# Kernel optimization log

Measured on AMD Instinct MI355X. Metric: run time of the kernel, lower is better.

## Reference

```python
import math
import jax, jax.numpy as jnp
import numpy as np

B, C_IN, H, W = 32, 96, 64, 64
OUT = 128
EXC = int(OUT * 0.8)   # 102 excitatory channels
INH = OUT - EXC        # 26 inhibitory channels
K = 5
PAD = 2                # kernel//2 so all stages keep spatial size


def _sm_kernel(kernel_size=5, sigma_e=1.2, sigma_i=1.4):
    c = kernel_size // 2
    xx, yy = np.meshgrid(np.arange(kernel_size), np.arange(kernel_size), indexing='ij')
    xx = xx.astype(np.float32) - c
    yy = yy.astype(np.float32) - c
    ge = np.exp(-(xx ** 2 + yy ** 2) / (2 * sigma_e ** 2))
    gi = np.exp(-(xx ** 2 + yy ** 2) / (2 * sigma_i ** 2))
    dog = ge / (2 * math.pi * sigma_e ** 2) - gi / (2 * math.pi * sigma_i ** 2)
    dog = dog / dog[c, c]
    return jnp.asarray(dog[None, None], dtype=jnp.float32)  # [1,1,K,K]


def setup_inputs() -> dict:
    key = jax.random.key(0)
    k1, k2, k3, k4 = jax.random.split(key, 4)
    wr = 25.0 / math.sqrt(C_IN * K * K)
    x = jax.random.normal(k1, (B, C_IN, H, W), jnp.float32)
    w_ee = wr * jnp.abs(jax.random.normal(k2, (EXC, C_IN, K, K), jnp.float32))
    w_ei = wr * jnp.abs(jax.random.normal(k3, (INH, EXC, K, K), jnp.float32))
    w_ie = -wr * jnp.abs(jax.random.normal(k4, (EXC, INH, K, K), jnp.float32))
    return {"x": x, "w_ee": w_ee, "w_ei": w_ei, "w_ie": w_ie, "sm_kernel": _sm_kernel()}


def _reflect_pad(x, p):
    if p == 0:
        return x
    return jnp.pad(x, ((0, 0), (0, 0), (p, p), (p, p)), mode='reflect')


def _conv(x, w, pad=0, groups=1):
    return jax.lax.conv_general_dilated(
        x, w, window_strides=(1, 1), padding=[(pad, pad), (pad, pad)],
        dimension_numbers=('NCHW', 'OIHW', 'NCHW'), feature_group_count=groups)


def _forward(x, w_ee, w_ei, w_ie, sm_kernel):
    y_e = _conv(_reflect_pad(x, PAD), w_ee)                 # [B,EXC,H,W], act=Identity
    y_i = jax.nn.relu(_conv(_reflect_pad(y_e, PAD), w_ei))  # [B,INH,H,W]
    y_ie = _conv(_reflect_pad(y_i, PAD), w_ie)              # [B,EXC,H,W]
    y = y_e + y_ie
    # depthwise surround-modulation conv (zero padding, as in F.conv2d)
    w_sm = jnp.tile(sm_kernel, (EXC, 1, 1, 1))              # [EXC,1,K,K]
    y = _conv(y, w_sm, pad=K // 2, groups=EXC)
    return y, y_e, y_i


def reference(x, w_ee, w_ei, w_ie, sm_kernel):
    y, y_e, y_i = _forward(x, w_ee, w_ei, w_ie, sm_kernel)

    # --- hard WTA masks (winner channel per (b,h,w) position) ---
    win_e = jnp.argmax(y_e, axis=1)                                        # [B,H,W]
    mask_e = (jnp.arange(EXC)[None, :, None, None] == win_e[:, None]).astype(y_e.dtype)
    y_wta_e = y_e * mask_e
    win_i = jnp.argmax(jnp.abs(y_i), axis=1)
    mask_i = (jnp.arange(INH)[None, :, None, None] == win_i[:, None]).astype(y_i.dtype)
    y_wta_i = y_i * mask_i

    # --- transpose-conv outer-product trick; with same-size feature maps the
    # conv collapses to a 1x1 full correlation over (b,h,w) -> einsum ---
    yx_ee = jnp.einsum('bchw,behw->ec', x, y_wta_e)[:, :, None, None]      # [EXC,C_IN,1,1]
    yx_ei = jnp.einsum('behw,bihw->ie', y_wta_e, y_wta_i)[:, :, None, None]  # [INH,EXC,1,1]
    yx_ie = jnp.einsum('bihw,behw->ei', y_wta_i, y)[:, :, None, None]      # [EXC,INH,1,1]

    yu_e = jnp.sum(y_wta_e, axis=(0, 2, 3))[:, None, None, None]           # [EXC,1,1,1]
    yu_i = jnp.sum(jnp.abs(y_wta_i), axis=(0, 2, 3))[:, None, None, None]  # [INH,1,1,1]

    upd_ee = yx_ee - yu_e * w_ee   # broadcasts to [EXC,C_IN,K,K]
    upd_ei = yx_ei - yu_i * w_ei
    upd_ie = yx_ie - yu_e * w_ie
    upd_ee = upd_ee / (jnp.abs(upd_ee).max() + 1e-8)
    upd_ei = upd_ei / (jnp.abs(upd_ei).max() + 1e-8)
    upd_ie = upd_ie / (jnp.abs(upd_ie).max() + 1e-8)

    return (y, upd_ee, upd_ei, upd_ie)
```

## Files before the change

### kernel.cpp

```cpp
#include <hip/hip_runtime.h>

#define B_    32
#define CIN_  96
#define EXC_  102
#define INH_  26
#define HH    64
#define WW    64
#define HW_   4096
#define NPOS  (B_*HW_)
#define EEPAD 97
#define NPART 1024
#define NEE   (EXC_*CIN_ + EXC_)
#define NIE   (EXC_*INH_)
#define N1U   (EXC_*CIN_*25)
#define N2U   (INH_*EXC_*25)
#define N3U   (EXC_*INH_*25)

typedef short bf8 __attribute__((ext_vector_type(8)));
typedef float f32x4 __attribute__((ext_vector_type(4)));

__device__ __forceinline__ int refl(int i) {
    if (i < 0) i = -i;
    if (i > 63) i = 126 - i;
    return i;
}

__device__ __forceinline__ short f2bf(float f) {
    unsigned u = __float_as_uint(f);
    return (short)((u + 0x7fffu + ((u >> 16) & 1u)) >> 16);
}

__global__ __launch_bounds__(256) void pack_all(
    const float* __restrict__ w_ee, const float* __restrict__ w_ei,
    const float* __restrict__ w_ie, const float* __restrict__ x,
    short* __restrict__ wdst, short* __restrict__ xdst,
    float* __restrict__ zreg)
{
    const int blk = blockIdx.x;
    if (blk < 1800) {
        int gi = blk*256 + threadIdx.x;
        if (gi >= 460800) return;
        const float* src; int N, C, NPAD, CPAD; int idx;
        if (gi < 268800)      { src = w_ee; N = 102; C = 96;  NPAD = 112; CPAD = 96;  idx = gi; }
        else if (gi < 371200) { src = w_ei; N = 26;  C = 102; NPAD = 32;  CPAD = 128; idx = gi - 268800; }
        else                  { src = w_ie; N = 102; C = 26;  NPAD = 112; CPAD = 32;  idx = gi - 371200; }
        int tap = idx / (NPAD*CPAD);
        int rem = idx - tap*(NPAD*CPAD);
        int n = rem / CPAD, c = rem - n*CPAD;
        float f = (n < N && c < C) ? src[((size_t)n*C + c)*25 + tap] : 0.f;
        wdst[gi] = f2bf(f);
    } else if (blk < 3848) {
        int bb = blk - 1800;
        int b = bb >> 6, bx = bb & 63;
        const int pos = bx*64 + (threadIdx.x & 63);
        const int cg0 = threadIdx.x >> 6;
        for (int cg = cg0; cg < 96/8; cg += 4) {
            bf8 v;
#pragma unroll
            for (int j = 0; j < 8; ++j)
                v[j] = f2bf(x[((size_t)b*CIN_ + cg*8 + j)*HW_ + pos]);
            *(bf8*)(&xdst[((size_t)b*HW_ + pos)*96 + cg*8]) = v;
        }
    } else {
        for (int i = threadIdx.x; i < INH_*EXC_ + INH_ + 3; i += 256) zreg[i] = 0.f;
    }
}

template<int C, int CPAD>
__global__ __launch_bounds__(256) void pack_nhwc(
    const float* __restrict__ src, short* __restrict__ dst)
{
    const int b = blockIdx.z;
    const int pos = blockIdx.x*64 + (threadIdx.x & 63);
    const int cg0 = threadIdx.x >> 6;
    for (int cg = cg0; cg < CPAD/8; cg += 4) {
        bf8 v;
#pragma unroll
        for (int j = 0; j < 8; ++j) {
            int c = cg*8 + j;
            float f = (c < C) ? src[((size_t)b*C + c)*HW_ + pos] : 0.f;
            v[j] = f2bf(f);
        }
        *(bf8*)(&dst[((size_t)b*HW_ + pos)*CPAD + cg*8]) = v;
    }
}

template<int CPAD, int NPAD, int NT, int COUT, int NCHUNK,
         bool RELU, bool ADDIN, bool WFLOAT, int OCPAD, bool WTA>
__global__ __launch_bounds__(256, 2) void conv_mfma(
    const short* __restrict__ src, const short* __restrict__ wgt,
    const float* __restrict__ addin, float* __restrict__ out,
    short* __restrict__ nhwc_out, int* __restrict__ win,
    float* __restrict__ val)
{
    __shared__ __align__(16) short sA[400*40];
    const int t  = threadIdx.x;
    const int bx = blockIdx.x;
    const int b  = blockIdx.z;
    const int h0 = (bx >> 2) * 16;
    const int w0 = (bx &  3) * 16;
    const int lane = t & 63;
    const int wv = t >> 6;
    const int nh = lane & 15;
    const int q  = lane >> 4;

    int goff[7], loff[7];
#pragma unroll
    for (int s = 0; s < 7; ++s) {
        int i = t + 256*s;
        if (i < 1600) {
            int rec = i >> 2, seg = i & 3;
            int lh = rec / 20, lw = rec - lh*20;
            int gh = refl(h0 - 2 + lh), gw = refl(w0 - 2 + lw);
            goff[s] = (b*HW_ + gh*WW + gw) * CPAD + seg*8;
            loff[s] = rec*40 + seg*8;
        } else { goff[s] = 0; loff[s] = -1; }
    }

    f32x4 acc[4][NT];
#pragma unroll
    for (int mt = 0; mt < 4; ++mt)
#pragma unroll
        for (int nt = 0; nt < NT; ++nt) {
            f32x4 z = {0.f, 0.f, 0.f, 0.f};
            acc[mt][nt] = z;
        }

    int abase[4];
#pragma unroll
    for (int mt = 0; mt < 4; ++mt)
        abase[mt] = ((wv*4 + mt)*20 + nh)*40 + q*8;

    for (int ck = 0; ck < NCHUNK; ++ck) {
        const int c0 = ck*32;
        __syncthreads();
#pragma unroll
        for (int s = 0; s < 7; ++s)
            if (loff[s] >= 0)
                *(bf8*)(&sA[loff[s]]) = *(const bf8*)(&src[goff[s] + c0]);
        __syncthreads();
        const short* wch = wgt + c0 + nh*CPAD + q*8;
        for (int dh = 0; dh < 5; ++dh) {
#pragma unroll
            for (int dw = 0; dw < 5; ++dw) {
                const int tap = dh*5 + dw;
                bf8 bfr[NT];
#pragma unroll
                for (int nt = 0; nt < NT; ++nt)
                    bfr[nt] = *(const bf8*)(&wch[(size_t)(tap*NPAD + nt*16)*CPAD]);
                bf8 afr[4];
#pragma unroll
                for (int mt = 0; mt < 4; ++mt)
                    afr[mt] = *(const bf8*)(&sA[abase[mt] + (dh*20 + dw)*40]);
#pragma unroll
                for (int mt = 0; mt < 4; ++mt)
#pragma unroll
                    for (int nt = 0; nt < NT; ++nt)
                        acc[mt][nt] = __builtin_amdgcn_mfma_f32_16x16x32_bf16(
                            afr[mt], bfr[nt], acc[mt][nt], 0, 0, 0);
            }
        }
    }

#pragma unroll
    for (int mt = 0; mt < 4; ++mt) {
        const int rowi = h0 + wv*4 + mt;
#pragma unroll
        for (int nt = 0; nt < NT; ++nt) {
            const int chn = nt*16 + nh;
            if (WFLOAT && chn < COUT) {
                size_t obase = ((size_t)(b*COUT + chn))*HW_ + rowi*WW + w0 + q*4;
#pragma unroll
                for (int r = 0; r < 4; ++r) {
                    float v = acc[mt][nt][r];
                    if (RELU) v = fmaxf(v, 0.f);
                    if (ADDIN) v += addin[obase + r];
                    out[obase + r] = v;
                }
            }
            if (OCPAD > 0) {
#pragma unroll
                for (int r = 0; r < 4; ++r) {
                    float v = acc[mt][nt][r];
                    if (RELU) v = fmaxf(v, 0.f);
                    int pos = rowi*WW + w0 + q*4 + r;
                    nhwc_out[((size_t)b*HW_ + pos)*OCPAD + chn] = f2bf(v);
                }
            }
        }
        if (OCPAD > NT*16) {
#pragma unroll
            for (int r = 0; r < 4; ++r) {
                int pos = rowi*WW + w0 + q*4 + r;
                for (int ct = NT*16 + nh; ct < OCPAD; ct += 16)
                    nhwc_out[((size_t)b*HW_ + pos)*OCPAD + ct] = 0;
            }
        }
        if (WTA) {
#pragma unroll
            for (int r = 0; r < 4; ++r) {
                float bv = -3.402823e38f; int bc = 0;
#pragma unroll
                for (int nt = 0; nt < NT; ++nt) {
                    const int chn = nt*16 + nh;
                    float v = acc[mt][nt][r];
                    if (RELU) v = fmaxf(v, 0.f);
                    if (chn < COUT && v > bv) { bv = v; bc = chn; }
                }
#pragma unroll
                for (int off = 1; off < 16; off <<= 1) {
                    float ov = __shfl_xor(bv, off);
                    int   oc = __shfl_xor(bc, off);
                    if (ov > bv || (ov == bv && oc < bc)) { bv = ov; bc = oc; }
                }
                if (nh == 0) {
                    int p = b*HW_ + rowi*WW + w0 + q*4 + r;
                    win[p] = bc; val[p] = bv;
                }
            }
        }
    }
}

__global__ __launch_bounds__(256) void smconv_v2(
    const float* __restrict__ in, const float* __restrict__ sm,
    float* __restrict__ out)
{
    __shared__ __align__(16) float sx[36*36];
    const int tid = threadIdx.x;
    const int tile = blockIdx.x;
    const int e = blockIdx.y;
    const int b = blockIdx.z;
    const int h0 = (tile >> 1) * 32, w0 = (tile & 1) * 32;
    const int r  = tid >> 3;
    const int cg = (tid & 7) * 4;
    const float* inc = in + ((size_t)(b*EXC_ + e))*HW_;
#pragma unroll
    for (int it = 0; it < 6; ++it) {
        int i = tid + it*256;
        if (i < 1296) {
            int lh = i / 36, lw = i - lh*36;
            int gh = h0 - 2 + lh, gw = w0 - 2 + lw;
            float v = 0.f;
            if (gh >= 0 && gh < HH && gw >= 0 && gw < WW) v = inc[gh*WW + gw];
            sx[i] = v;
        }
    }
    __syncthreads();
    float a0 = 0.f, a1 = 0.f, a2 = 0.f, a3 = 0.f;
#pragma unroll
    for (int kh = 0; kh < 5; ++kh) {
        const float4* rowp = (const float4*)(sx + (r + kh)*36 + cg);
        float4 v0 = rowp[0], v1 = rowp[1];
        float xv[8] = {v0.x, v0.y, v0.z, v0.w, v1.x, v1.y, v1.z, v1.w};
#pragma unroll
        for (int kw = 0; kw < 5; ++kw) {
            float wv = sm[kh*5 + kw];
            a0 = fmaf(xv[kw+0], wv, a0);
            a1 = fmaf(xv[kw+1], wv, a1);
            a2 = fmaf(xv[kw+2], wv, a2);
            a3 = fmaf(xv[kw+3], wv, a3);
        }
    }
    size_t oidx = ((size_t)(b*EXC_ + e))*HW_ + (h0 + r)*WW + w0 + cg;
    *(float4*)(out + oidx) = make_float4(a0, a1, a2, a3);
}

__global__ __launch_bounds__(256) void scatter_ee_kernel(
    const float* __restrict__ x, const int* __restrict__ win_e,
    const float* __restrict__ val_e, float* __restrict__ parts)
{
    __shared__ float s_yx[EXC_*EEPAD];
    __shared__ float s_yu[EXC_];
    for (int i = threadIdx.x; i < EXC_*EEPAD; i += 256) s_yx[i] = 0.f;
    if (threadIdx.x < EXC_) s_yu[threadIdx.x] = 0.f;
    __syncthreads();
    const int pos_i = threadIdx.x & 127;
    const int half  = threadIdx.x >> 7;
    int p = blockIdx.x * 128 + pos_i;
    int b = p >> 12, hw = p & 4095;
    int wi = win_e[p]; float v = val_e[p];
    if (half == 0) atomicAdd(&s_yu[wi], v);
    const float* xb = x + ((size_t)b*CIN_ + half*48)*HW_ + hw;
    float* row = s_yx + wi*EEPAD + half*48;
    for (int c = 0; c < 48; ++c)
        atomicAdd(&row[c], v * xb[(size_t)c*HW_]);
    __syncthreads();
    float* dst = parts + (size_t)blockIdx.x * NEE;
    for (int i = threadIdx.x; i < EXC_*CIN_; i += 256) {
        int e = i / CIN_, c = i - e*CIN_;
        dst[i] = s_yx[e*EEPAD + c];
    }
    if (threadIdx.x < EXC_) dst[EXC_*CIN_ + threadIdx.x] = s_yu[threadIdx.x];
}

__global__ __launch_bounds__(256) void scatter_iei_kernel(
    const float* __restrict__ y, const int* __restrict__ win_e,
    const float* __restrict__ val_e, const int* __restrict__ win_i,
    const float* __restrict__ val_i, float* __restrict__ yx_ei,
    float* __restrict__ yu_i, float* __restrict__ parts)
{
    __shared__ float s_ei[INH_*EXC_ + INH_];
    __shared__ float s_ie[EXC_*INH_];
    for (int i = threadIdx.x; i < INH_*EXC_ + INH_; i += 256) s_ei[i] = 0.f;
    for (int i = threadIdx.x; i < EXC_*INH_; i += 256) s_ie[i] = 0.f;
    __syncthreads();
    const int pos_i = threadIdx.x & 127;
    const int half  = threadIdx.x >> 7;
    int p = blockIdx.x * 128 + pos_i;
    int b = p >> 12, hw = p & 4095;
    int wi = win_i[p]; float vi = val_i[p];
    if (half == 0) {
        int we = win_e[p]; float ve = val_e[p];
        atomicAdd(&s_ei[wi*EXC_ + we], ve*vi);
        atomicAdd(&s_ei[INH_*EXC_ + wi], fabsf(vi));
    }
    if (vi != 0.f) {
        const float* yb = y + ((size_t)b*EXC_ + half*51)*HW_ + hw;
        float* se = s_ie + half*51*INH_ + wi;
        for (int e = 0; e < 51; ++e)
            atomicAdd(&se[e*INH_], vi * yb[(size_t)e*HW_]);
    }
    __syncthreads();
    for (int i = threadIdx.x; i < INH_*EXC_ + INH_; i += 256) {
        float v = s_ei[i];
        if (v != 0.f) {
            if (i < INH_*EXC_) atomicAdd(&yx_ei[i], v);
            else               atomicAdd(&yu_i[i - INH_*EXC_], v);
        }
    }
    float* dst = parts + (size_t)blockIdx.x * NIE;
    for (int i = threadIdx.x; i < EXC_*INH_; i += 256) dst[i] = s_ie[i];
}

__global__ __launch_bounds__(256) void reduce_all_kernel(
    const float* __restrict__ parts_ee, const float* __restrict__ parts_ie,
    float* __restrict__ yx_ee, float* __restrict__ yx_ie)
{
    __shared__ float s[256];
    int col = blockIdx.x*64 + (threadIdx.x & 63);
    int g = threadIdx.x >> 6;
    const float* P; float* D; int n, i;
    if (col < NEE) { P = parts_ee; D = yx_ee; n = NEE; i = col; }
    else           { P = parts_ie; D = yx_ie; n = NIE; i = col - NEE; }
    float a = 0.f;
    if (col < NEE + NIE) {
        for (int j = g*(NPART/4); j < (g+1)*(NPART/4); ++j)
            a += P[(size_t)j*n + i];
    }
    s[threadIdx.x] = a;
    __syncthreads();
    if (threadIdx.x < 64 && col < NEE + NIE)
        D[i] = s[threadIdx.x] + s[threadIdx.x+64] + s[threadIdx.x+128] + s[threadIdx.x+192];
}

__global__ __launch_bounds__(256) void upd_absmax3(
    const float* __restrict__ yx_ee, const float* __restrict__ yu_e,
    const float* __restrict__ w_ee,
    const float* __restrict__ yx_ei, const float* __restrict__ yu_i,
    const float* __restrict__ w_ei,
    const float* __restrict__ yx_ie, const float* __restrict__ w_ie,
    unsigned int* __restrict__ amax)
{
    float m0 = 0.f, m1 = 0.f, m2 = 0.f;
    for (int idx = blockIdx.x*256 + threadIdx.x; idx < N1U + N2U + N3U;
         idx += gridDim.x*256) {
        if (idx < N1U) {
            int ec = idx / 25; int e = ec / CIN_;
            m0 = fmaxf(m0, fabsf(yx_ee[ec] - yu_e[e]*w_ee[idx]));
        } else if (idx < N1U + N2U) {
            int j = idx - N1U; int ec = j / 25; int e = ec / EXC_;
            m1 = fmaxf(m1, fabsf(yx_ei[ec] - yu_i[e]*w_ei[j]));
        } else {
            int j = idx - N1U - N2U; int ec = j / 25; int e = ec / INH_;
            m2 = fmaxf(m2, fabsf(yx_ie[ec] - yu_e[e]*w_ie[j]));
        }
    }
    __shared__ unsigned int s0, s1, s2;
    if (threadIdx.x == 0) { s0 = 0u; s1 = 0u; s2 = 0u; }
    __syncthreads();
    atomicMax(&s0, __float_as_uint(m0));
    atomicMax(&s1, __float_as_uint(m1));
    atomicMax(&s2, __float_as_uint(m2));
    __syncthreads();
    if (threadIdx.x == 0) {
        atomicMax(&amax[0], s0);
        atomicMax(&amax[1], s1);
        atomicMax(&amax[2], s2);
    }
}

__global__ __launch_bounds__(256) void upd_write3(
    const float* __restrict__ yx_ee, const float* __restrict__ yu_e,
    const float* __restrict__ w_ee,
    const float* __restrict__ yx_ei, const float* __restrict__ yu_i,
    const float* __restrict__ w_ei,
    const float* __restrict__ yx_ie, const float* __restrict__ w_ie,
    const unsigned int* __restrict__ amax,
    float* __restrict__ out_ee, float* __restrict__ out_ei,
    float* __restrict__ out_ie)
{
    int idx = blockIdx.x*256 + threadIdx.x;
    if (idx >= N1U + N2U + N3U) return;
    if (idx < N1U) {
        int ec = idx / 25; int e = ec / CIN_;
        float v = yx_ee[ec] - yu_e[e]*w_ee[idx];
        out_ee[idx] = v / (__uint_as_float(amax[0]) + 1e-8f);
    } else if (idx < N1U + N2U) {
        int j = idx - N1U; int ec = j / 25; int e = ec / EXC_;
        float v = yx_ei[ec] - yu_i[e]*w_ei[j];
        out_ei[j] = v / (__uint_as_float(amax[1]) + 1e-8f);
    } else {
        int j = idx - N1U - N2U; int ec = j / 25; int e = ec / INH_;
        float v = yx_ie[ec] - yu_e[e]*w_ie[j];
        out_ie[j] = v / (__uint_as_float(amax[2]) + 1e-8f);
    }
}

extern "C" void kernel_launch(void* const* d_in, const int* in_sizes, int n_in,
                              void* d_out, int out_size, void* d_ws, size_t ws_size,
                              hipStream_t stream)
{
    const float* x    = (const float*)d_in[0];
    const float* w_ee = (const float*)d_in[1];
    const float* w_ei = (const float*)d_in[2];
    const float* w_ie = (const float*)d_in[3];
    const float* smk  = (const float*)d_in[4];
    float* out = (float*)d_out;

    const size_t SZ_YE   = (size_t)B_*EXC_*HW_;
    const size_t SZ_YEBF = (size_t)B_*HW_*128;
    const size_t SZ_XBF  = (size_t)B_*HW_*96;
    const size_t SZ_W    = 460800;
    const size_t need_direct =
        SZ_YE*4 + SZ_YEBF*2 + SZ_XBF*2 + SZ_W*2 + (size_t)NPOS*16 + 16000*4;
    const bool direct = (ws_size >= need_direct);

    float* y_e  = (float*)d_ws;
    short* yebf; short* R;
    if (direct) {
        yebf = (short*)(y_e + SZ_YE);
        R    = yebf + SZ_YEBF;
    } else {
        yebf = nullptr;
        R    = (short*)(y_e + SZ_YE);
    }
    short* yibf = direct ? R : R;
    short* bigR = direct ? R : (R + (size_t)B_*HW_*32);
    short* wee  = direct ? (R + SZ_XBF) : (bigR + (size_t)16777216);
    short* wei  = wee + 268800;
    short* wie  = wei + 102400;
    int*   win_e = (int*)(wie + 89600);
    float* val_e = (float*)(win_e + NPOS);
    int*   win_i = (int*)(val_e + NPOS);
    float* val_i = (float*)(win_i + NPOS);
    float* yx_ee = val_i + NPOS;
    float* yu_e  = yx_ee + EXC_*CIN_;
    float* yx_ie = yu_e + EXC_;
    float* yx_ei = yx_ie + EXC_*INH_;
    float* yu_i  = yx_ei + INH_*EXC_;
    unsigned int* amax = (unsigned int*)(yu_i + INH_);
    float* parts_ee = y_e;
    float* parts_ie = parts_ee + (size_t)NPART*NEE;

    pack_all<<<3849, 256, 0, stream>>>(w_ee, w_ei, w_ie, x, wee, bigR, yx_ei);

    if (direct) {
        conv_mfma<96, 112, 7, EXC_, 3, false, false, true, 128, true>
            <<<dim3(16, 1, B_), 256, 0, stream>>>(bigR, wee, nullptr, y_e, yebf,
                                                  win_e, val_e);
        conv_mfma<128, 32, 2, INH_, 4, true, false, false, 32, true>
            <<<dim3(16, 1, B_), 256, 0, stream>>>(yebf, wei, nullptr, nullptr,
                                                  yibf, win_i, val_i);
        conv_mfma<32, 112, 7, EXC_, 1, false, true, true, 0, false>
            <<<dim3(16, 1, B_), 256, 0, stream>>>(yibf, wie, y_e, y_e, nullptr,
                                                  nullptr, nullptr);
    } else {
        conv_mfma<96, 112, 7, EXC_, 3, false, false, true, 0, true>
            <<<dim3(16, 1, B_), 256, 0, stream>>>(bigR, wee, nullptr, y_e, nullptr,
                                                  win_e, val_e);
        pack_nhwc<EXC_, 128><<<dim3(64, 1, B_), 256, 0, stream>>>(y_e, bigR);
        conv_mfma<128, 32, 2, INH_, 4, true, false, false, 32, true>
            <<<dim3(16, 1, B_), 256, 0, stream>>>(bigR, wei, nullptr, nullptr,
                                                  yibf, win_i, val_i);
        conv_mfma<32, 112, 7, EXC_, 1, false, true, true, 0, false>
            <<<dim3(16, 1, B_), 256, 0, stream>>>(yibf, wie, y_e, y_e, nullptr,
                                                  nullptr, nullptr);
    }

    smconv_v2<<<dim3(4, EXC_, B_), 256, 0, stream>>>(y_e, smk, out);

    scatter_ee_kernel<<<NPART, 256, 0, stream>>>(x, win_e, val_e, parts_ee);
    scatter_iei_kernel<<<NPART, 256, 0, stream>>>(out, win_e, val_e, win_i,
                                                  val_i, yx_ei, yu_i, parts_ie);

    reduce_all_kernel<<<(NEE + NIE + 63)/64, 256, 0, stream>>>(
        parts_ee, parts_ie, yx_ee, yx_ie);

    upd_absmax3<<<480, 256, 0, stream>>>(yx_ee, yu_e, w_ee, yx_ei, yu_i, w_ei,
                                         yx_ie, w_ie, amax);
    float* out_ee = out + (size_t)B_*EXC_*HW_;
    float* out_ei = out_ee + N1U;
    float* out_ie = out_ei + N2U;
    upd_write3<<<(N1U + N2U + N3U + 255)/256, 256, 0, stream>>>(
        yx_ee, yu_e, w_ee, yx_ei, yu_i, w_ei, yx_ie, w_ie, amax,
        out_ee, out_ei, out_ie);
}
```

Baseline: 580.1 us.

## Stage activation tiles in LDS and reassign threads to channels in WTA scatter kernels

The two winner-take-all scatter kernels now handle 256 positions per block instead of 128, which halves the number of partial-sum blocks. Each block stages 32-position chunks of x or y into padded shared memory with float4 loads, and each thread owns one channel while looping over positions. This replaces strided per-position global loads and scattered row atomics with coalesced loads and channel-indexed shared atomics, and it halves the partial buffers that the reduction kernel must sum. The cost is extra barriers per chunk and atomic contention on the same winner row across threads.

```diff
diff --git a/kernel.cpp b/kernel.cpp
--- a/kernel.cpp
+++ b/kernel.cpp
@@ -8,8 +8,7 @@
 #define WW    64
 #define HW_   4096
 #define NPOS  (B_*HW_)
-#define EEPAD 97
-#define NPART 1024
+#define NPART 512
 #define NEE   (EXC_*CIN_ + EXC_)
 #define NIE   (EXC_*INH_)
 #define N1U   (EXC_*CIN_*25)
@@ -270,28 +269,53 @@
     const float* __restrict__ x, const int* __restrict__ win_e,
     const float* __restrict__ val_e, float* __restrict__ parts)
 {
-    __shared__ float s_yx[EXC_*EEPAD];
+    __shared__ float s_yx[EXC_*CIN_];
     __shared__ float s_yu[EXC_];
-    for (int i = threadIdx.x; i < EXC_*EEPAD; i += 256) s_yx[i] = 0.f;
-    if (threadIdx.x < EXC_) s_yu[threadIdx.x] = 0.f;
-    __syncthreads();
-    const int pos_i = threadIdx.x & 127;
-    const int half  = threadIdx.x >> 7;
-    int p = blockIdx.x * 128 + pos_i;
-    int b = p >> 12, hw = p & 4095;
-    int wi = win_e[p]; float v = val_e[p];
-    if (half == 0) atomicAdd(&s_yu[wi], v);
-    const float* xb = x + ((size_t)b*CIN_ + half*48)*HW_ + hw;
-    float* row = s_yx + wi*EEPAD + half*48;
-    for (int c = 0; c < 48; ++c)
-        atomicAdd(&row[c], v * xb[(size_t)c*HW_]);
-    __syncthreads();
-    float* dst = parts + (size_t)blockIdx.x * NEE;
-    for (int i = threadIdx.x; i < EXC_*CIN_; i += 256) {
-        int e = i / CIN_, c = i - e*CIN_;
-        dst[i] = s_yx[e*EEPAD + c];
-    }
-    if (threadIdx.x < EXC_) dst[EXC_*CIN_ + threadIdx.x] = s_yu[threadIdx.x];
+    __shared__ float s_xs[CIN_*33];
+    __shared__ float s_val[256];
+    __shared__ int   s_win[256];
+    const int t = threadIdx.x;
+    for (int i = t; i < EXC_*CIN_; i += 256) s_yx[i] = 0.f;
+    if (t < EXC_) s_yu[t] = 0.f;
+    {
+        int p = blockIdx.x*256 + t;
+        s_win[t] = win_e[p];
+        s_val[t] = val_e[p];
+    }
+    const int p0  = blockIdx.x * 256;
+    const int b   = p0 >> 12;
+    const int hw0 = p0 & 4095;
+    const float* xb = x + (size_t)b*CIN_*HW_ + hw0;
+    const int c = (t < 96) ? t : t - 96;
+    const int h = (t < 96) ? 0 : 1;
+
+    for (int ch = 0; ch < 8; ++ch) {
+        __syncthreads();
+#pragma unroll
+        for (int it = 0; it < 3; ++it) {
+            int idx = t + it*256;
+            if (idx < 768) {
+                int cr = idx >> 3, c4 = idx & 7;
+                float4 v = *(const float4*)(xb + (size_t)cr*HW_ + ch*32 + c4*4);
+                float* d = &s_xs[cr*33 + c4*4];
+                d[0] = v.x; d[1] = v.y; d[2] = v.z; d[3] = v.w;
+            }
+        }
+        __syncthreads();
+        if (t < 192) {
+#pragma unroll
+            for (int k = 0; k < 16; ++k) {
+                int pos = ch*32 + h*16 + k;
+                float ve = s_val[pos]; int we = s_win[pos];
+                atomicAdd(&s_yx[we*CIN_ + c], ve * s_xs[c*33 + h*16 + k]);
+                if (c == 0) atomicAdd(&s_yu[we], ve);
+            }
+        }
+    }
+    __syncthreads();
+    float* dee = parts + (size_t)blockIdx.x * NEE;
+    for (int i = t; i < EXC_*CIN_; i += 256) dee[i] = s_yx[i];
+    if (t < EXC_) dee[EXC_*CIN_ + t] = s_yu[t];
 }
 
 __global__ __launch_bounds__(256) void scatter_iei_kernel(
@@ -300,37 +324,75 @@
     const float* __restrict__ val_i, float* __restrict__ yx_ei,
     float* __restrict__ yu_i, float* __restrict__ parts)
 {
+    __shared__ float s_ie[EXC_*27];
     __shared__ float s_ei[INH_*EXC_ + INH_];
-    __shared__ float s_ie[EXC_*INH_];
-    for (int i = threadIdx.x; i < INH_*EXC_ + INH_; i += 256) s_ei[i] = 0.f;
-    for (int i = threadIdx.x; i < EXC_*INH_; i += 256) s_ie[i] = 0.f;
-    __syncthreads();
-    const int pos_i = threadIdx.x & 127;
-    const int half  = threadIdx.x >> 7;
-    int p = blockIdx.x * 128 + pos_i;
-    int b = p >> 12, hw = p & 4095;
-    int wi = win_i[p]; float vi = val_i[p];
-    if (half == 0) {
+    __shared__ float s_ys[EXC_*33];
+    __shared__ float s_val[256];
+    __shared__ int   s_win[256];
+    const int t = threadIdx.x;
+    for (int i = t; i < EXC_*27; i += 256) s_ie[i] = 0.f;
+    for (int i = t; i < INH_*EXC_ + INH_; i += 256) s_ei[i] = 0.f;
+    {
+        int p = blockIdx.x*256 + t;
+        s_win[t] = win_i[p];
+        s_val[t] = val_i[p];
+    }
+    __syncthreads();
+
+    {
+        int p = blockIdx.x*256 + t;
         int we = win_e[p]; float ve = val_e[p];
+        int wi = s_win[t]; float vi = s_val[t];
         atomicAdd(&s_ei[wi*EXC_ + we], ve*vi);
         atomicAdd(&s_ei[INH_*EXC_ + wi], fabsf(vi));
     }
-    if (vi != 0.f) {
-        const float* yb = y + ((size_t)b*EXC_ + half*51)*HW_ + hw;
-        float* se = s_ie + half*51*INH_ + wi;
-        for (int e = 0; e < 51; ++e)
-            atomicAdd(&se[e*INH_], vi * yb[(size_t)e*HW_]);
-    }
-    __syncthreads();
-    for (int i = threadIdx.x; i < INH_*EXC_ + INH_; i += 256) {
+
+    const int p0  = blockIdx.x * 256;
+    const int b   = p0 >> 12;
+    const int hw0 = p0 & 4095;
+    const float* yb = y + (size_t)b*EXC_*HW_ + hw0;
+    const int e = (t < 102) ? t : t - 102;
+    const int h = (t < 102) ? 0 : 1;
+
+    for (int ch = 0; ch < 8; ++ch) {
+        __syncthreads();
+#pragma unroll
+        for (int it = 0; it < 4; ++it) {
+            int idx = t + it*256;
+            if (idx < 816) {
+                int er = idx >> 3, c4 = idx & 7;
+                float4 v = *(const float4*)(yb + (size_t)er*HW_ + ch*32 + c4*4);
+                float* d = &s_ys[er*33 + c4*4];
+                d[0] = v.x; d[1] = v.y; d[2] = v.z; d[3] = v.w;
+            }
+        }
+        __syncthreads();
+        if (t < 204) {
+#pragma unroll
+            for (int k = 0; k < 16; ++k) {
+                int pos = ch*32 + h*16 + k;
+                float vi = s_val[pos];
+                if (vi != 0.f) {
+                    int wi = s_win[pos];
+                    atomicAdd(&s_ie[e*27 + wi], vi * s_ys[e*33 + h*16 + k]);
+                }
+            }
+        }
+    }
+    __syncthreads();
+
+    for (int i = t; i < INH_*EXC_ + INH_; i += 256) {
         float v = s_ei[i];
         if (v != 0.f) {
             if (i < INH_*EXC_) atomicAdd(&yx_ei[i], v);
             else               atomicAdd(&yu_i[i - INH_*EXC_], v);
         }
     }
-    float* dst = parts + (size_t)blockIdx.x * NIE;
-    for (int i = threadIdx.x; i < EXC_*INH_; i += 256) dst[i] = s_ie[i];
+    float* die = parts + (size_t)blockIdx.x * NIE;
+    for (int i = t; i < EXC_*INH_; i += 256) {
+        int ee = i / INH_, ii = i - ee*INH_;
+        die[i] = s_ie[ee*27 + ii];
+    }
 }
 
 __global__ __launch_bounds__(256) void reduce_all_kernel(
```

After: 561.0 us. 3.3% less time.
